# Optimization experiments

Hardware: AMD Instinct MI355X
Metric: run time of the kernel (lower is better)

The kernel has to match this reference:

```python
import jax, jax.numpy as jnp
import numpy as np

B, S, D, H = 2, 2048, 1024, 16
DK = D // H

def setup_inputs() -> dict:
    key = jax.random.key(0)
    ks = jax.random.split(key, 11)
    scale = 0.02
    inp = {
        "Q": jax.random.normal(ks[0], (B, S, D), jnp.float32),
        "K": jax.random.normal(ks[1], (B, S, D), jnp.float32),
        "V": jax.random.normal(ks[2], (B, S, D), jnp.float32),
        "mask": jnp.ones((B, S), jnp.int32),
        "Wq": jax.random.normal(ks[3], (D, D), jnp.float32) * scale,
        "bq": jnp.zeros((D,), jnp.float32),
        "Wk": jax.random.normal(ks[4], (D, D), jnp.float32) * scale,
        "bk": jnp.zeros((D,), jnp.float32),
        "Wv": jax.random.normal(ks[5], (D, D), jnp.float32) * scale,
        "bv": jnp.zeros((D,), jnp.float32),
        "Wo": jax.random.normal(ks[6], (D, D), jnp.float32) * scale,
        "bo": jnp.zeros((D,), jnp.float32),
    }
    return inp

def _split_heads(x):
    # [B,S,D] -> [B,H,S,DK]
    return x.reshape(B, S, H, DK).transpose(0, 2, 1, 3)

def reference(Q, K, V, mask, Wq, bq, Wk, bk, Wv, bv, Wo, bo):
    q = _split_heads(Q @ Wq.T + bq)
    k = _split_heads(K @ Wk.T + bk)
    v = _split_heads(V @ Wv.T + bv)
    scores = jnp.einsum("bhqd,bhkd->bhqk", q, k) / jnp.sqrt(jnp.float32(DK))
    # 2D padding mask -> [B,1,1,S], mask==0 positions set to -inf
    m = mask[:, None, None, :]
    scores = jnp.where(m == 0, -jnp.inf, scores)
    attn_weights = jax.nn.softmax(scores, axis=-1)  # [B,H,S,S]
    attn_output = jnp.einsum("bhqk,bhkd->bhqd", attn_weights, v)
    attn_output = attn_output.transpose(0, 2, 1, 3).reshape(B, S, D)
    output = attn_output @ Wo.T + bo
    return (output, attn_weights)
```

## Files before the change

### kernel.cpp

```cpp
#include <hip/hip_runtime.h>
#include <stdint.h>

#define DEVINL __device__ __forceinline__

typedef float  f32x4  __attribute__((ext_vector_type(4)));
typedef float  f32x16 __attribute__((ext_vector_type(16)));
typedef short  s16x8  __attribute__((ext_vector_type(8)));
typedef unsigned short u16x4 __attribute__((ext_vector_type(4)));
typedef unsigned short u16x8 __attribute__((ext_vector_type(8)));

static constexpr int S = 2048, D = 1024, H = 16;
static constexpr size_t OUT0 = (size_t)2 * S * D;

DEVINL unsigned short f2bf(float f) {
  union { float f; unsigned u; } v; v.f = f;
  unsigned r = v.u + 0x7FFFu + ((v.u >> 16) & 1u);
  return (unsigned short)(r >> 16);
}

DEVINL unsigned cvt_pk_bf16(float lo, float hi) {
  unsigned r;
  asm("v_cvt_pk_bf16_f32 %0, %1, %2" : "=v"(r) : "v"(lo), "v"(hi));
  return r;
}

DEVINL void perm32swap(unsigned& a, unsigned& b) {
#if __has_builtin(__builtin_amdgcn_permlane32_swap)
  auto r = __builtin_amdgcn_permlane32_swap(a, b, false, false);
  a = r[0]; b = r[1];
#else
  asm volatile("v_permlane32_swap_b32 %0, %1" : "+v"(a), "+v"(b));
#endif
}

DEVINL void gload_lds16(const void* g, void* l) {
  __builtin_amdgcn_global_load_lds(
      (const __attribute__((address_space(1))) unsigned int*)g,
      (__attribute__((address_space(3))) unsigned int*)l, 16, 0, 0);
}

DEVINL void cvt_body(const float* __restrict__ src, unsigned short* __restrict__ dst, int i) {
  const f32x4* s4 = (const f32x4*)src;
  f32x4 a = s4[i * 2], b = s4[i * 2 + 1];
  u16x8 o;
  o[0] = f2bf(a[0]); o[1] = f2bf(a[1]); o[2] = f2bf(a[2]); o[3] = f2bf(a[3]);
  o[4] = f2bf(b[0]); o[5] = f2bf(b[1]); o[6] = f2bf(b[2]); o[7] = f2bf(b[3]);
  ((u16x8*)dst)[i] = o;
}

__global__ __launch_bounds__(256) void k_cvt_all(
    const float* __restrict__ Q, const float* __restrict__ K, const float* __restrict__ V,
    const float* __restrict__ Wq, const float* __restrict__ Wk,
    const float* __restrict__ Wv, const float* __restrict__ Wo,
    unsigned short* __restrict__ Xq, unsigned short* __restrict__ Xk,
    unsigned short* __restrict__ Xv,
    unsigned short* __restrict__ WQ, unsigned short* __restrict__ WK,
    unsigned short* __restrict__ WV, unsigned short* __restrict__ WO) {
  int i = blockIdx.x;
  const float* src; unsigned short* dst; int item;
  if (i < 6144) {
    int z = i >> 11;
    item = (i & 2047) * 256 + threadIdx.x;
    src = z == 0 ? Q : z == 1 ? K : V;
    dst = z == 0 ? Xq : z == 1 ? Xk : Xv;
  } else {
    int j = i - 6144, z = j >> 9;
    item = (j & 511) * 256 + threadIdx.x;
    src = z == 0 ? Wq : z == 1 ? Wk : z == 2 ? Wv : Wo;
    dst = z == 0 ? WQ : z == 1 ? WK : z == 2 ? WV : WO;
  }
  cvt_body(src, dst, item);
}

template <int MODE>
DEVINL void gemm_tile(const unsigned short* __restrict__ A,
                      const unsigned short* __restrict__ Bw,
                      const float* __restrict__ bias, void* __restrict__ Cout,
                      int tileM, int tileN, float scl, char* smem) {
  unsigned short* As = (unsigned short*)smem;
  unsigned short* Bs = (unsigned short*)(smem + 8192);
  const int tid = threadIdx.x;
  const int lane = tid & 63, wave = tid >> 6;
  const int wr = wave >> 1, wc = wave & 1;
  const int l15 = lane & 15, l16 = lane >> 4;
  f32x4 acc[4][4] = {};
  for (int k0 = 0; k0 < 1024; k0 += 32) {
#pragma unroll
    for (int p = 0; p < 2; ++p) {
      int c = tid + p * 256;
      int row = c >> 2, col = (c & 3) * 8;
      gload_lds16(A + (((size_t)(tileM + row)) << 10) + k0 + col, &As[c * 8]);
      gload_lds16(Bw + (((size_t)(tileN + row)) << 10) + k0 + col, &Bs[c * 8]);
    }
    __syncthreads();
    s16x8 af[4], bf[4];
#pragma unroll
    for (int i = 0; i < 4; ++i)
      af[i] = *(const s16x8*)&As[(wr * 64 + i * 16 + l15) * 32 + l16 * 8];
#pragma unroll
    for (int i = 0; i < 4; ++i)
      bf[i] = *(const s16x8*)&Bs[(wc * 64 + i * 16 + l15) * 32 + l16 * 8];
#pragma unroll
    for (int i = 0; i < 4; ++i)
#pragma unroll
      for (int j = 0; j < 4; ++j)
        acc[i][j] = __builtin_amdgcn_mfma_f32_16x16x32_bf16(af[i], bf[j], acc[i][j], 0, 0, 0);
    __syncthreads();
  }

  if (MODE == 2) {
    unsigned short* T = (unsigned short*)smem;
#pragma unroll
    for (int i = 0; i < 4; ++i)
#pragma unroll
      for (int j = 0; j < 4; ++j) {
        int n = wc * 64 + j * 16 + l15;
        float bv = bias[tileN + n];
        int m0 = wr * 64 + i * 16 + l16 * 4;
        u16x4 o;
#pragma unroll
        for (int r = 0; r < 4; ++r) o[r] = f2bf(acc[i][j][r] + bv);
        *(u16x4*)((char*)T + n * 256 + ((m0 * 2) ^ ((n & 15) << 4))) = o;
      }
    __syncthreads();
    {
      int n = tid >> 1, mh = tid & 1;
      int d = (tileN + n) & 63, h_ = (tileN + n) >> 6;
      int b_ = tileM >> 11;
      int kt_ = (((tileM & 2047) + mh * 64) >> 6);
      unsigned short* dst = (unsigned short*)Cout + (size_t)(b_ * H + h_) * S * 64 +
                            (size_t)kt_ * 4096 + d * 64;
#pragma unroll
      for (int k = 0; k < 8; ++k) {
        int mc = mh * 64 + k * 8;
        u16x8 v = *(const u16x8*)((const char*)T + n * 256 + ((mc * 2) ^ ((n & 15) << 4)));
        *(u16x8*)(dst + k * 8) = v;
      }
    }
  } else {
#pragma unroll
    for (int i = 0; i < 4; ++i) {
#pragma unroll
      for (int j = 0; j < 4; ++j) {
        int n = tileN + wc * 64 + j * 16 + l15;
        float bv = bias[n];
#pragma unroll
        for (int r = 0; r < 4; ++r) {
          int m = tileM + wr * 64 + i * 16 + l16 * 4 + r;
          float v = (acc[i][j][r] + bv) * scl;
          if (MODE == 0) {
            int b_ = m >> 11, s_ = m & 2047, h_ = n >> 6, d_ = n & 63;
            ((unsigned short*)Cout)[(((size_t)(b_ * H + h_) * S) + s_) * 64 + d_] = f2bf(v);
          } else {
            ((float*)Cout)[(size_t)m * 1024 + n] = v;
          }
        }
      }
    }
  }
}

__global__ __launch_bounds__(256) void k_gemm_qkv(
    const unsigned short* __restrict__ Xq, const unsigned short* __restrict__ Xk,
    const unsigned short* __restrict__ Xv,
    const unsigned short* __restrict__ Wq, const unsigned short* __restrict__ Wk,
    const unsigned short* __restrict__ Wv,
    const float* __restrict__ bq, const float* __restrict__ bk, const float* __restrict__ bv,
    unsigned short* __restrict__ oq, unsigned short* __restrict__ ok,
    unsigned short* __restrict__ vt2) {
  __shared__ alignas(16) char smem[32768];
  int flat = (blockIdx.z * 32 + blockIdx.y) * 8 + blockIdx.x;
  int swz = (flat & 7) * 96 + (flat >> 3);
  int z = swz >> 8;
  int rem = swz & 255;
  int ty = rem >> 3, tx = rem & 7;
  if (z == 2) {
    gemm_tile<2>(Xv, Wv, bv, vt2, ty * 128, tx * 128, 1.0f, smem);
  } else {
    const unsigned short* A = z == 0 ? Xq : Xk;
    const unsigned short* W = z == 0 ? Wq : Wk;
    const float* bias = z == 0 ? bq : bk;
    unsigned short* o = z == 0 ? oq : ok;
    gemm_tile<0>(A, W, bias, o, ty * 128, tx * 128, z == 0 ? 0.125f : 1.0f, smem);
  }
}

__global__ __launch_bounds__(256) void k_gemm_out(const unsigned short* __restrict__ A,
                                                  const unsigned short* __restrict__ W,
                                                  const float* __restrict__ bias,
                                                  float* __restrict__ Cout) {
  __shared__ alignas(16) char smem[16384];
  int flat = blockIdx.y * 8 + blockIdx.x;
  int swz = (flat & 7) * 32 + (flat >> 3);
  int ty = swz >> 3, tx = swz & 7;
  gemm_tile<1>(A, W, bias, Cout, ty * 128, tx * 128, 1.0f, smem);
}

__global__ __launch_bounds__(256) void k_attn_fused(const unsigned short* __restrict__ qw,
                                                    const unsigned short* __restrict__ kw,
                                                    const unsigned short* __restrict__ vt2,
                                                    const int* __restrict__ mask,
                                                    unsigned short* __restrict__ aout,
                                                    float* __restrict__ attw) {
  __shared__ alignas(16) char lds[33792];
  float* lsumW = (float*)(lds + 32768);
  float* lsumT = (float*)(lds + 33280);
  float* nl2lW = (float*)(lds + 33536);
  const float LOG2E = 1.44269504f;

  int flat = blockIdx.y * 32 + blockIdx.x;
  int swzb = (flat & 7) * 128 + (flat >> 3);
  const int bh = swzb >> 5, b = bh >> 4, h = bh & 15;
  const int q0 = (swzb & 31) * 64;
  const int tid = threadIdx.x;
  const int lane = tid & 63, w = tid >> 6;
  const int l31 = lane & 31, hi = lane >> 5;
  const int qg = w >> 1, kb = w & 1;

  const unsigned short* kw_bh = kw + (size_t)bh * S * 64;
  const unsigned short* vt_bh = vt2 + (size_t)bh * S * 64;
  const int* mrow = mask + b * S;

  s16x8 qf[4];
  const unsigned short* qbase = qw + ((size_t)bh * S + q0 + qg * 32 + l31) * 64 + hi * 8;
#pragma unroll
  for (int kc = 0; kc < 4; ++kc) qf[kc] = *(const s16x8*)(qbase + kc * 16);

  f32x16 oT0 = {}, oT1 = {};
  float lsum = 0.f;
  const int swv = (l31 & 7) << 4;

#pragma unroll
  for (int p = 0; p < 2; ++p) {
    int c = tid + p * 256, row = c >> 3, cc = (c & 7) ^ (row & 7);
    gload_lds16(kw_bh + (size_t)row * 64 + cc * 8, lds + c * 16);
    gload_lds16(vt_bh + (size_t)row * 64 + cc * 8, lds + 16384 + c * 16);
  }
  __syncthreads();

  int cur = 0;
  for (int t = 0; t < 32; ++t) {
    if (t + 1 < 32) {
      int nt = t + 1;
      int nxt = (cur ^ 1) * 8192;
#pragma unroll
      for (int p = 0; p < 2; ++p) {
        int c = tid + p * 256, row = c >> 3, cc = (c & 7) ^ (row & 7);
        gload_lds16(kw_bh + ((size_t)(nt * 64 + row)) * 64 + cc * 8, lds + nxt + c * 16);
        gload_lds16(vt_bh + (size_t)nt * 4096 + row * 64 + cc * 8, lds + 16384 + nxt + c * 16);
      }
    }
    const char* Kc = lds + cur * 8192;
    const char* Vc = lds + 16384 + cur * 8192;

    const int krow = kb * 32 + l31;
    f32x16 sT = {};
#pragma unroll
    for (int kc = 0; kc < 4; ++kc) {
      s16x8 ka = *(const s16x8*)(Kc + krow * 128 +
                                 ((kc * 32 + hi * 16) ^ ((krow & 7) << 4)));
      sT = __builtin_amdgcn_mfma_f32_32x32x16_bf16(ka, qf[kc], sT, 0, 0, 0);
    }

    int base = t * 64 + kb * 32 + 4 * hi;
    int m[16];
    *(int4*)&m[0]  = *(const int4*)&mrow[base];
    *(int4*)&m[4]  = *(const int4*)&mrow[base + 8];
    *(int4*)&m[8]  = *(const int4*)&mrow[base + 16];
    *(int4*)&m[12] = *(const int4*)&mrow[base + 24];

    float e[16];
#pragma unroll
    for (int r = 0; r < 16; ++r) {
      e[r] = m[r] ? exp2f(sT[r] * LOG2E) : 0.f;
      lsum += e[r];
    }

    unsigned x0 = cvt_pk_bf16(e[0], e[1]),   x1 = cvt_pk_bf16(e[2], e[3]);
    unsigned x2 = cvt_pk_bf16(e[4], e[5]),   x3 = cvt_pk_bf16(e[6], e[7]);
    unsigned x4 = cvt_pk_bf16(e[8], e[9]),   x5 = cvt_pk_bf16(e[10], e[11]);
    unsigned x6 = cvt_pk_bf16(e[12], e[13]), x7 = cvt_pk_bf16(e[14], e[15]);
    perm32swap(x0, x2); perm32swap(x1, x3);
    perm32swap(x4, x6); perm32swap(x5, x7);
    union { unsigned u[4]; s16x8 v; } p0u, p1u;
    p0u.u[0] = x0; p0u.u[1] = x1; p0u.u[2] = x2; p0u.u[3] = x3;
    p1u.u[0] = x4; p1u.u[1] = x5; p1u.u[2] = x6; p1u.u[3] = x7;

    const int ko0 = kb * 64 + hi * 16, ko1 = kb * 64 + 32 + hi * 16;
    const char* Vr0 = Vc + l31 * 128;
    const char* Vr1 = Vc + (32 + l31) * 128;
    s16x8 va;
    va = *(const s16x8*)(Vr0 + (ko0 ^ swv));
    oT0 = __builtin_amdgcn_mfma_f32_32x32x16_bf16(va, p0u.v, oT0, 0, 0, 0);
    va = *(const s16x8*)(Vr0 + (ko1 ^ swv));
    oT0 = __builtin_amdgcn_mfma_f32_32x32x16_bf16(va, p1u.v, oT0, 0, 0, 0);
    va = *(const s16x8*)(Vr1 + (ko0 ^ swv));
    oT1 = __builtin_amdgcn_mfma_f32_32x32x16_bf16(va, p0u.v, oT1, 0, 0, 0);
    va = *(const s16x8*)(Vr1 + (ko1 ^ swv));
    oT1 = __builtin_amdgcn_mfma_f32_32x32x16_bf16(va, p1u.v, oT1, 0, 0, 0);

    __syncthreads();
    cur ^= 1;
  }

  lsum += __shfl_xor(lsum, 32);
  if (hi == 0) lsumW[w * 32 + l31] = lsum;

  const int sqq = (l31 & 15) << 4;
  {
    char* orow = lds + w * 8192 + l31 * 256;
#pragma unroll
    for (int rg = 0; rg < 4; ++rg) {
      f32x4 c0, c1;
#pragma unroll
      for (int j = 0; j < 4; ++j) { c0[j] = oT0[rg * 4 + j]; c1[j] = oT1[rg * 4 + j]; }
      *(f32x4*)(orow + ((rg * 32 + hi * 16) ^ sqq)) = c0;
      *(f32x4*)(orow + ((128 + rg * 32 + hi * 16) ^ sqq)) = c1;
    }
  }
  __syncthreads();

  if (tid < 64) {
    int qg_ = tid >> 5, qq = tid & 31;
    float tot = lsumW[qg_ * 64 + qq] + lsumW[qg_ * 64 + 32 + qq];
    lsumT[tid] = tot;
    nl2lW[tid] = __log2f(tot);
  }
  __syncthreads();

  {
    int q = tid >> 2, dq = tid & 3;
    int qg_ = q >> 5, qq = q & 31;
    float inv = 1.f / lsumT[q];
    int sq = (qq & 15) << 4;
    float s[16] = {};
#pragma unroll
    for (int w2 = 0; w2 < 2; ++w2) {
      const char* prow = lds + (qg_ * 2 + w2) * 8192 + qq * 256;
#pragma unroll
      for (int c = 0; c < 4; ++c) {
        f32x4 a = *(const f32x4*)(prow + ((dq * 64 + c * 16) ^ sq));
#pragma unroll
        for (int j = 0; j < 4; ++j) s[c * 4 + j] += a[j];
      }
    }
    u16x8 ob0, ob1;
#pragma unroll
    for (int j = 0; j < 8; ++j) { ob0[j] = f2bf(s[j] * inv); ob1[j] = f2bf(s[8 + j] * inv); }
    unsigned short* abase = aout + ((size_t)b * S + q0 + q) * D + h * 64 + dq * 16;
    *(u16x8*)abase = ob0;
    *(u16x8*)(abase + 8) = ob1;
  }

  float nl2l[16];
#pragma unroll
  for (int r = 0; r < 16; ++r) nl2l[r] = nl2lW[qg * 32 + (r & 3) + 8 * (r >> 2) + 4 * hi];

  for (int it = 0; it < 32; ++it) {
    int key0 = it * 64 + kb * 32;
    const unsigned short* kbase = kw_bh + (size_t)(key0 + l31) * 64 + hi * 8;
    s16x8 kfr[4];
#pragma unroll
    for (int kc = 0; kc < 4; ++kc) kfr[kc] = *(const s16x8*)(kbase + kc * 16);
    f32x16 dacc = {};
#pragma unroll
    for (int kc = 0; kc < 4; ++kc)
      dacc = __builtin_amdgcn_mfma_f32_32x32x16_bf16(qf[kc], kfr[kc], dacc, 0, 0, 0);

    int key = key0 + l31;
    int mk = mrow[key];
    float* obase = attw + ((size_t)bh * S + q0 + qg * 32) * S + key;
#pragma unroll
    for (int r = 0; r < 16; ++r) {
      int row = (r & 3) + 8 * (r >> 2) + 4 * hi;
      float wv = mk ? exp2f(dacc[r] * LOG2E - nl2l[r]) : 0.f;
      __builtin_nontemporal_store(wv, obase + (size_t)row * S);
    }
  }
}

extern "C" void kernel_launch(void* const* d_in, const int* in_sizes, int n_in,
                              void* d_out, int out_size, void* d_ws, size_t ws_size,
                              hipStream_t stream) {
  (void)in_sizes; (void)n_in; (void)out_size; (void)ws_size;
  const float* Q  = (const float*)d_in[0];
  const float* K  = (const float*)d_in[1];
  const float* V  = (const float*)d_in[2];
  const int* mask = (const int*)d_in[3];
  const float* Wq = (const float*)d_in[4];
  const float* bq = (const float*)d_in[5];
  const float* Wk = (const float*)d_in[6];
  const float* bk = (const float*)d_in[7];
  const float* Wv = (const float*)d_in[8];
  const float* bv = (const float*)d_in[9];
  const float* Wo = (const float*)d_in[10];
  const float* bo = (const float*)d_in[11];

  char* ws = (char*)d_ws;
  unsigned short* Xbf  = (unsigned short*)(ws + 0);
  unsigned short* Wbf  = (unsigned short*)(ws + 25165824);
  unsigned short* qws  = (unsigned short*)(ws + 33554432);
  unsigned short* kws  = (unsigned short*)(ws + 41943040);
  unsigned short* vt2  = (unsigned short*)(ws + 50331648);
  unsigned short* aoutb= (unsigned short*)(ws + 8388608);
  float* out0 = (float*)d_out;
  float* attw = (float*)d_out + OUT0;

  k_cvt_all<<<dim3(8192), dim3(256), 0, stream>>>(
      Q, K, V, Wq, Wk, Wv, Wo,
      Xbf, Xbf + 4194304, Xbf + 8388608,
      Wbf, Wbf + 1048576, Wbf + 2097152, Wbf + 3145728);

  k_gemm_qkv<<<dim3(8, 32, 3), dim3(256), 0, stream>>>(
      Xbf, Xbf + 4194304, Xbf + 8388608,
      Wbf, Wbf + 1048576, Wbf + 2097152,
      bq, bk, bv, qws, kws, vt2);

  k_attn_fused<<<dim3(32, 32), dim3(256), 0, stream>>>(qws, kws, vt2, mask, aoutb, attw);

  k_gemm_out<<<dim3(8, 32), dim3(256), 0, stream>>>(aoutb, Wbf + 3145728, bo, out0);
}
```

Before: 234.5 us.

## Double-buffer GEMM LDS tiles and stage Q/K epilogue through LDS

The GEMM main loop now double-buffers its A/B tiles in LDS, issuing the global-to-LDS loads for the next k-slice before computing on the current one. This removes one barrier per iteration and overlaps load latency with MFMA work. The Q/K projection epilogue (MODE 0) now writes bf16 results into a swizzled LDS tile and then stores 16-byte vectors to the head-split layout, replacing scattered 2-byte global stores. The output GEMM kernel's shared memory doubles to 32 KB to hold both buffers, which may reduce occupancy.

```diff
diff --git a/kernel.cpp b/kernel.cpp
--- a/kernel.cpp
+++ b/kernel.cpp
@@ -77,22 +77,35 @@
                       const unsigned short* __restrict__ Bw,
                       const float* __restrict__ bias, void* __restrict__ Cout,
                       int tileM, int tileN, float scl, char* smem) {
-  unsigned short* As = (unsigned short*)smem;
-  unsigned short* Bs = (unsigned short*)(smem + 8192);
   const int tid = threadIdx.x;
   const int lane = tid & 63, wave = tid >> 6;
   const int wr = wave >> 1, wc = wave & 1;
   const int l15 = lane & 15, l16 = lane >> 4;
   f32x4 acc[4][4] = {};
+
+#pragma unroll
+  for (int p = 0; p < 2; ++p) {
+    int c = tid + p * 256;
+    int row = c >> 2, col = (c & 3) * 8;
+    gload_lds16(A + (((size_t)(tileM + row)) << 10) + col, smem + c * 16);
+    gload_lds16(Bw + (((size_t)(tileN + row)) << 10) + col, smem + 8192 + c * 16);
+  }
+  __syncthreads();
+
+  int cur = 0;
   for (int k0 = 0; k0 < 1024; k0 += 32) {
-#pragma unroll
-    for (int p = 0; p < 2; ++p) {
-      int c = tid + p * 256;
-      int row = c >> 2, col = (c & 3) * 8;
-      gload_lds16(A + (((size_t)(tileM + row)) << 10) + k0 + col, &As[c * 8]);
-      gload_lds16(Bw + (((size_t)(tileN + row)) << 10) + k0 + col, &Bs[c * 8]);
-    }
-    __syncthreads();
+    if (k0 + 32 < 1024) {
+      int nxt = (cur ^ 1) * 16384;
+#pragma unroll
+      for (int p = 0; p < 2; ++p) {
+        int c = tid + p * 256;
+        int row = c >> 2, col = (c & 3) * 8;
+        gload_lds16(A + (((size_t)(tileM + row)) << 10) + k0 + 32 + col, smem + nxt + c * 16);
+        gload_lds16(Bw + (((size_t)(tileN + row)) << 10) + k0 + 32 + col, smem + nxt + 8192 + c * 16);
+      }
+    }
+    const unsigned short* As = (const unsigned short*)(smem + cur * 16384);
+    const unsigned short* Bs = (const unsigned short*)(smem + cur * 16384 + 8192);
     s16x8 af[4], bf[4];
 #pragma unroll
     for (int i = 0; i < 4; ++i)
@@ -106,9 +119,39 @@
       for (int j = 0; j < 4; ++j)
         acc[i][j] = __builtin_amdgcn_mfma_f32_16x16x32_bf16(af[i], bf[j], acc[i][j], 0, 0, 0);
     __syncthreads();
-  }
-
-  if (MODE == 2) {
+    cur ^= 1;
+  }
+
+  if (MODE == 0) {
+    unsigned short* T = (unsigned short*)smem;
+#pragma unroll
+    for (int i = 0; i < 4; ++i)
+#pragma unroll
+      for (int j = 0; j < 4; ++j) {
+        int n = wc * 64 + j * 16 + l15;
+        float bv = bias[tileN + n];
+#pragma unroll
+        for (int r = 0; r < 4; ++r) {
+          int m = wr * 64 + i * 16 + l16 * 4 + r;
+          *(unsigned short*)((char*)T + m * 256 + ((n * 2) ^ ((m & 15) << 4))) =
+              f2bf((acc[i][j][r] + bv) * scl);
+        }
+      }
+    __syncthreads();
+    {
+      int mr = tid >> 1, half = tid & 1;
+      int m = tileM + mr;
+      int b_ = m >> 11, s_ = m & 2047;
+      int h_ = ((tileN + half * 64) >> 6);
+      unsigned short* dst = (unsigned short*)Cout + ((size_t)(b_ * H + h_) * S + s_) * 64;
+#pragma unroll
+      for (int k = 0; k < 8; ++k) {
+        u16x8 v = *(const u16x8*)((const char*)T + mr * 256 +
+                                  ((half * 128 + k * 16) ^ ((mr & 15) << 4)));
+        *(u16x8*)(dst + k * 8) = v;
+      }
+    }
+  } else if (MODE == 2) {
     unsigned short* T = (unsigned short*)smem;
 #pragma unroll
     for (int i = 0; i < 4; ++i)
@@ -147,13 +190,7 @@
 #pragma unroll
         for (int r = 0; r < 4; ++r) {
           int m = tileM + wr * 64 + i * 16 + l16 * 4 + r;
-          float v = (acc[i][j][r] + bv) * scl;
-          if (MODE == 0) {
-            int b_ = m >> 11, s_ = m & 2047, h_ = n >> 6, d_ = n & 63;
-            ((unsigned short*)Cout)[(((size_t)(b_ * H + h_) * S) + s_) * 64 + d_] = f2bf(v);
-          } else {
-            ((float*)Cout)[(size_t)m * 1024 + n] = v;
-          }
+          ((float*)Cout)[(size_t)m * 1024 + n] = (acc[i][j][r] + bv) * scl;
         }
       }
     }
@@ -189,7 +226,7 @@
                                                   const unsigned short* __restrict__ W,
                                                   const float* __restrict__ bias,
                                                   float* __restrict__ Cout) {
-  __shared__ alignas(16) char smem[16384];
+  __shared__ alignas(16) char smem[32768];
   int flat = blockIdx.y * 8 + blockIdx.x;
   int swz = (flat & 7) * 32 + (flat >> 3);
   int ty = swz >> 3, tx = swz & 7;
```

Result: no change. 230.4 us, median of 2 (-1.7%).
